# Kernel optimization log

Hardware: AMD Instinct MI355X
Metric: run time of the kernel (lower is better)

The kernel has to match this reference:

```python
import jax, jax.numpy as jnp
import numpy as np
from jax import lax


def setup_inputs() -> dict:
    key = jax.random.key(0)
    k1, k2 = jax.random.split(key)
    B, N, D = 4, 4096, 128
    f_s = jax.random.normal(k1, (B, N, D), dtype=jnp.float32)
    f_trans = jax.random.normal(k2, (B, N, D), dtype=jnp.float32)
    return {"f_s": f_s, "f_trans": f_trans}


def reference(f_s, f_trans):
    temp = 10.0
    eps = 1e-8
    B, N, D = f_s.shape
    # pairwise dot products, reused for cosine sim and for the logits ("all")
    dots = jnp.einsum('bnd,bmd->bnm', f_s, f_trans)  # [B,N,M]
    norm_s = jnp.linalg.norm(f_s, axis=-1)       # [B,N]
    norm_t = jnp.linalg.norm(f_trans, axis=-1)   # [B,M]
    # torch.cosine_similarity: dot / max(|x|*|y|, eps)
    sim = dots / jnp.maximum(norm_s[:, :, None] * norm_t[:, None, :], eps)
    # argmax over dim=1 (the N axis) -> index per (b, m)
    idx = jnp.argmax(sim, axis=1)  # [B,M] int
    # gather f_trans rows at those indices (detached in the original via numpy)
    pos_q_trans = lax.stop_gradient(
        jnp.take_along_axis(f_trans, idx[..., None], axis=1))  # [B,M,D]
    pos_logit = jnp.sum(f_s * pos_q_trans, axis=-1) / temp  # [B,N] (N==M)
    pos_exp = jnp.exp(pos_logit)
    # sum_m exp(<f_s_n, f_trans_m>/temp) without materializing [B,N,M,D]
    all_exp = jnp.sum(jnp.exp(dots / temp), axis=-1)  # [B,N]
    ratio = jnp.clip(pos_exp / all_exp, 1e-40)
    loss = jnp.mean(jnp.sum(-jnp.log(ratio), axis=-1) / N)
    return loss
```

## Files before the change

kernel.cpp:

```cpp
#include <hip/hip_runtime.h>
#include <math.h>

#define BB 4
#define NN 4096
#define DD 128
#define MSPLIT 8
#define NIT 8
#define TM 64
#define NP 128

typedef __attribute__((ext_vector_type(8))) short bf16x8;
typedef __attribute__((ext_vector_type(4))) float f32x4;

__device__ __forceinline__ void mfma_16x16x32_bf16(f32x4& d, bf16x8 a, bf16x8 b) {
  asm volatile("v_mfma_f32_16x16x32_bf16 %0, %1, %2, %0" : "+v"(d) : "v"(a), "v"(b));
}

__device__ __forceinline__ void gload16(const void* g, void* lds) {
  __builtin_amdgcn_global_load_lds(
      (const __attribute__((address_space(1))) void*)g,
      (__attribute__((address_space(3))) void*)lds, 16, 0, 0);
}

__device__ __forceinline__ unsigned short f2b(float x) {
  union { float f; unsigned u; } v; v.f = x;
  unsigned r = v.u + 0x7fffu + ((v.u >> 16) & 1u);
  return (unsigned short)(r >> 16);
}

__global__ __launch_bounds__(256) void k_prep(const float* __restrict__ fs,
                                              const float* __restrict__ ft,
                                              unsigned* __restrict__ outb,
                                              float* __restrict__ inv_norm) {
  int w = threadIdx.x >> 6, lane = threadIdx.x & 63;
  int row = blockIdx.x * 4 + w;
  bool is_s = row < BB * NN;
  const float* src = is_s ? fs + (size_t)row * DD
                          : ft + ((size_t)row - BB * NN) * DD;
  float2 v = ((const float2*)src)[lane];
  const float C = 0.14426950408889634f;
  float cx = is_s ? v.x : v.x * C;
  float cy = is_s ? v.y : v.y * C;
  outb[(size_t)row * 64 + lane] = ((unsigned)f2b(cy) << 16) | f2b(cx);
  if (is_s) {
    float s = v.x * v.x + v.y * v.y;
#pragma unroll
    for (int off = 32; off > 0; off >>= 1) s += __shfl_xor(s, off);
    if (lane == 0) inv_norm[row] = 1.0f / sqrtf(s);
  }
}

__global__ __launch_bounds__(256, 4) void k_main(const unsigned short* __restrict__ fsb,
                                                 const unsigned short* __restrict__ ftb,
                                                 const float* __restrict__ inv_norm,
                                                 float* __restrict__ psum,
                                                 float2* __restrict__ pmaxvi) {
  __shared__ __align__(16) char smem[32768];

  const int t = threadIdx.x;
  const int tn = blockIdx.x, h = blockIdx.y, b = blockIdx.z;
  const int w = t >> 6, lane = t & 63;
  const int l15 = lane & 15, g = lane >> 4;

  const int t16 = t >> 4, cp = t & 15;
  const int srcThr = t16 * 256 + ((cp ^ (t16 & 15)) << 4);
  const int ldsThr = w * 1024;

  const char* gA = (const char*)(fsb + ((size_t)b * NN + (size_t)tn * 128) * DD);
  const char* gB0 = (const char*)(ftb + ((size_t)b * NN + (size_t)h * (NIT * TM)) * DD);

#pragma unroll
  for (int p = 0; p < 8; p++)
    gload16(gA + p * 4096 + srcThr, smem + p * 4096 + ldsThr);
  __syncthreads();

  bf16x8 af[4][2];
#pragma unroll
  for (int kk = 0; kk < 4; kk++)
#pragma unroll
    for (int fi = 0; fi < 2; fi++) {
      int Ra = w * 32 + fi * 16 + l15;
      af[kk][fi] = *(const bf16x8*)(smem + Ra * 256 + (((kk * 4 + g) ^ l15) << 4));
    }
  float sv[2][4];
  int rowid[2][4];
  const float* invb = inv_norm + (size_t)b * NN + tn * 128 + w * 32 + g * 4;
#pragma unroll
  for (int fi = 0; fi < 2; fi++)
#pragma unroll
    for (int j = 0; j < 4; j++) {
      sv[fi][j] = invb[fi * 16 + j];
      rowid[fi][j] = w * 32 + fi * 16 + g * 4 + j;
    }
  __syncthreads();

  char* cb = smem;
  char* nb = smem + 16384;

#pragma unroll
  for (int p = 0; p < 4; p++)
    gload16(gB0 + p * 4096 + srcThr, cb + p * 4096 + ldsThr);

  float rowacc[2][4] = {};

  for (int it = 0; it < NIT; ++it) {
    __syncthreads();
    if (it + 1 < NIT) {
      const char* gBn = gB0 + (size_t)(it + 1) * (TM * DD * 2);
#pragma unroll
      for (int p = 0; p < 4; p++)
        gload16(gBn + p * 4096 + srcThr, nb + p * 4096 + ldsThr);
    }
    f32x4 acc[2][4] = {};
#pragma unroll
    for (int kk = 0; kk < 4; kk++) {
      bf16x8 bfr[4];
#pragma unroll
      for (int fj = 0; fj < 4; fj++) {
        int Rb = fj * 16 + l15;
        bfr[fj] = *(const bf16x8*)(cb + Rb * 256 + (((kk * 4 + g) ^ l15) << 4));
      }
#pragma unroll
      for (int fi = 0; fi < 2; fi++)
#pragma unroll
        for (int fj = 0; fj < 4; fj++)
          mfma_16x16x32_bf16(acc[fi][fj], af[kk][fi], bfr[fj]);
    }
#pragma unroll
    for (int fi = 0; fi < 2; fi++)
#pragma unroll
      for (int j = 0; j < 4; j++) {
        float s = (exp2f(acc[fi][0][j]) + exp2f(acc[fi][1][j])) +
                  (exp2f(acc[fi][2][j]) + exp2f(acc[fi][3][j]));
        rowacc[fi][j] += s;
      }
#pragma unroll
    for (int fj = 0; fj < 4; fj++) {
      float bv = -INFINITY; int bi = 0x7fffffff;
#pragma unroll
      for (int fi = 0; fi < 2; fi++)
#pragma unroll
        for (int j = 0; j < 4; j++) {
          float vv = acc[fi][fj][j] * sv[fi][j];
          if (vv > bv) { bv = vv; bi = rowid[fi][j]; }
        }
#pragma unroll
      for (int off = 16; off <= 32; off <<= 1) {
        float ov = __shfl_xor(bv, off);
        int   oi = __shfl_xor(bi, off);
        if (ov > bv || (ov == bv && oi < bi)) { bv = ov; bi = oi; }
      }
      if (g == 0) {
        int m = (h * NIT + it) * TM + fj * 16 + l15;
        float2 pr; pr.x = bv; pr.y = __int_as_float(tn * 128 + bi);
        pmaxvi[((size_t)b * NN + m) * NP + tn * 4 + w] = pr;
      }
    }
    char* tmp = cb; cb = nb; nb = tmp;
  }

#pragma unroll
  for (int fi = 0; fi < 2; fi++)
#pragma unroll
    for (int j = 0; j < 4; j++) {
      float s = rowacc[fi][j];
#pragma unroll
      for (int off = 1; off <= 8; off <<= 1) s += __shfl_xor(s, off);
      if (l15 == 0) {
        int n = tn * 128 + w * 32 + fi * 16 + g * 4 + j;
        psum[((size_t)b * NN + n) * MSPLIT + h] = s;
      }
    }
}

__global__ __launch_bounds__(256) void k_post(const float* __restrict__ fs,
                                              const float* __restrict__ ft,
                                              const float* __restrict__ psum,
                                              const float2* __restrict__ pmaxvi,
                                              float* __restrict__ blockpart) {
  __shared__ float part[4];
  int w = threadIdx.x >> 6, lane = threadIdx.x & 63;
  int row = blockIdx.x * 4 + w;
  int b = row >> 12;
  const float2* pp = pmaxvi + (size_t)row * NP;
  float2 p0 = pp[lane], p1 = pp[lane + 64];
  float v = p0.x; int i = __float_as_int(p0.y);
  {
    int i1 = __float_as_int(p1.y);
    if (p1.x > v || (p1.x == v && i1 < i)) { v = p1.x; i = i1; }
  }
#pragma unroll
  for (int off = 32; off > 0; off >>= 1) {
    float ov = __shfl_xor(v, off);
    int   oi = __shfl_xor(i, off);
    if (ov > v || (ov == v && oi < i)) { v = ov; i = oi; }
  }
  float2 a = ((const float2*)(fs + (size_t)row * DD))[lane];
  float2 c = ((const float2*)(ft + ((size_t)b * NN + i) * DD))[lane];
  float s = a.x * c.x + a.y * c.y;
#pragma unroll
  for (int off = 32; off > 0; off >>= 1) s += __shfl_xor(s, off);
  if (lane == 0) {
    const float4* ps4 = (const float4*)&psum[(size_t)row * MSPLIT];
    float4 q0 = ps4[0], q1 = ps4[1];
    float tot = ((q0.x + q0.y) + (q0.z + q0.w)) + ((q1.x + q1.y) + (q1.z + q1.w));
    float term = logf(tot) - s * 0.1f;
    part[w] = fminf(term, 92.103403719761827f);
  }
  __syncthreads();
  if (threadIdx.x == 0)
    blockpart[blockIdx.x] = part[0] + part[1] + part[2] + part[3];
}

__global__ __launch_bounds__(256) void k_final(const float* __restrict__ blockpart,
                                               float* __restrict__ out) {
  __shared__ float red[256];
  float s = 0.0f;
  for (int i = threadIdx.x; i < (BB * NN) / 4; i += 256) s += blockpart[i];
  red[threadIdx.x] = s;
  __syncthreads();
  for (int st = 128; st > 0; st >>= 1) {
    if (threadIdx.x < st) red[threadIdx.x] += red[threadIdx.x + st];
    __syncthreads();
  }
  if (threadIdx.x == 0) out[0] = red[0] * (1.0f / (BB * NN));
}

extern "C" void kernel_launch(void* const* d_in, const int* in_sizes, int n_in,
                              void* d_out, int out_size, void* d_ws, size_t ws_size,
                              hipStream_t stream) {
  const float* fs = (const float*)d_in[0];
  const float* ft = (const float*)d_in[1];
  float* out = (float*)d_out;

  const size_t NE = (size_t)BB * NN * DD;
  unsigned short* fsb = (unsigned short*)d_ws;
  unsigned short* ftb = fsb + NE;
  float*  inv_norm = (float*)(ftb + NE);
  float*  psum     = inv_norm + (size_t)BB * NN;
  float2* pmaxvi   = (float2*)(psum + (size_t)BB * NN * MSPLIT);
  float*  blockpart = (float*)(pmaxvi + (size_t)BB * NN * NP);

  k_prep<<<(2 * BB * NN) / 4, 256, 0, stream>>>(fs, ft, (unsigned*)fsb, inv_norm);
  dim3 g2(NN / 128, MSPLIT, BB);
  k_main<<<g2, 256, 0, stream>>>(fsb, ftb, inv_norm, psum, pmaxvi);
  k_post<<<(BB * NN) / 4, 256, 0, stream>>>(fs, ft, psum, pmaxvi, blockpart);
  k_final<<<1, 256, 0, stream>>>(blockpart, out);
}
```

Before: 65.76 us.

## Transpose main GEMM so argmax runs in-lane with packed index keys

Swaps the roles of the two operands so each wave owns 32 f_trans columns and scans f_s rows. The argmax over N is now a per-lane running fmax on a float key whose low 5 mantissa bits encode the tile position, which replaces the per-tile cross-lane shuffles and the wide partial-max buffer. Each wave reads operands straight from global memory without LDS staging or barriers. The exp-sum partials are written per 32-column group and reduced in the post kernel. The cost is more global and L2 traffic, no LDS reuse, and argmax ties resolved at reduced precision.

```diff
diff --git a/kernel.cpp b/kernel.cpp
--- a/kernel.cpp
+++ b/kernel.cpp
@@ -4,22 +4,15 @@
 #define BB 4
 #define NN 4096
 #define DD 128
-#define MSPLIT 8
+#define HS 8
 #define NIT 8
-#define TM 64
-#define NP 128
+#define MGROUPS 128
 
 typedef __attribute__((ext_vector_type(8))) short bf16x8;
 typedef __attribute__((ext_vector_type(4))) float f32x4;
 
 __device__ __forceinline__ void mfma_16x16x32_bf16(f32x4& d, bf16x8 a, bf16x8 b) {
   asm volatile("v_mfma_f32_16x16x32_bf16 %0, %1, %2, %0" : "+v"(d) : "v"(a), "v"(b));
-}
-
-__device__ __forceinline__ void gload16(const void* g, void* lds) {
-  __builtin_amdgcn_global_load_lds(
-      (const __attribute__((address_space(1))) void*)g,
-      (__attribute__((address_space(3))) void*)lds, 16, 0, 0);
 }
 
 __device__ __forceinline__ unsigned short f2b(float x) {
@@ -38,9 +31,8 @@
   const float* src = is_s ? fs + (size_t)row * DD
                           : ft + ((size_t)row - BB * NN) * DD;
   float2 v = ((const float2*)src)[lane];
-  const float C = 0.14426950408889634f;
-  float cx = is_s ? v.x : v.x * C;
-  float cy = is_s ? v.y : v.y * C;
+  float cx = is_s ? v.x : v.x * 0.1f;
+  float cy = is_s ? v.y : v.y * 0.1f;
   outb[(size_t)row * 64 + lane] = ((unsigned)f2b(cy) << 16) | f2b(cx);
   if (is_s) {
     float s = v.x * v.x + v.y * v.y;
@@ -54,121 +46,101 @@
                                                  const unsigned short* __restrict__ ftb,
                                                  const float* __restrict__ inv_norm,
                                                  float* __restrict__ psum,
-                                                 float2* __restrict__ pmaxvi) {
-  __shared__ __align__(16) char smem[32768];
-
+                                                 float2* __restrict__ pmax) {
   const int t = threadIdx.x;
-  const int tn = blockIdx.x, h = blockIdx.y, b = blockIdx.z;
   const int w = t >> 6, lane = t & 63;
   const int l15 = lane & 15, g = lane >> 4;
-
-  const int t16 = t >> 4, cp = t & 15;
-  const int srcThr = t16 * 256 + ((cp ^ (t16 & 15)) << 4);
-  const int ldsThr = w * 1024;
-
-  const char* gA = (const char*)(fsb + ((size_t)b * NN + (size_t)tn * 128) * DD);
-  const char* gB0 = (const char*)(ftb + ((size_t)b * NN + (size_t)h * (NIT * TM)) * DD);
-
-#pragma unroll
-  for (int p = 0; p < 8; p++)
-    gload16(gA + p * 4096 + srcThr, smem + p * 4096 + ldsThr);
-  __syncthreads();
-
+  const int gw = blockIdx.x * 4 + w;
+  const int b = gw >> 10;
+  const int h = (gw >> 7) & 7;
+  const int mg = gw & 127;
+  const int m0 = mg * 32;
+
+  const unsigned short* Abase = ftb + ((size_t)b * NN + m0) * DD;
   bf16x8 af[4][2];
 #pragma unroll
   for (int kk = 0; kk < 4; kk++)
 #pragma unroll
-    for (int fi = 0; fi < 2; fi++) {
-      int Ra = w * 32 + fi * 16 + l15;
-      af[kk][fi] = *(const bf16x8*)(smem + Ra * 256 + (((kk * 4 + g) ^ l15) << 4));
-    }
-  float sv[2][4];
-  int rowid[2][4];
-  const float* invb = inv_norm + (size_t)b * NN + tn * 128 + w * 32 + g * 4;
-#pragma unroll
-  for (int fi = 0; fi < 2; fi++)
+    for (int mf = 0; mf < 2; mf++)
+      af[kk][mf] = *(const bf16x8*)(Abase + (mf * 16 + l15) * DD + kk * 32 + g * 8);
+
+  const unsigned short* Ball = fsb + (size_t)b * NN * DD;
+  const float* invb = inv_norm + (size_t)b * NN;
+
+  float bkey[2][4];
+#pragma unroll
+  for (int mf = 0; mf < 2; mf++)
+#pragma unroll
+    for (int j = 0; j < 4; j++) bkey[mf][j] = 0.0f;
+
+#pragma unroll 1
+  for (int it = 0; it < NIT; ++it) {
+    const int n0 = h * 512 + it * 64;
+    float svn[4];
+#pragma unroll
+    for (int fj = 0; fj < 4; fj++) svn[fj] = invb[n0 + fj * 16 + l15];
+
+    f32x4 acc[2][4] = {};
+#pragma unroll
+    for (int kk = 0; kk < 4; kk++) {
+      bf16x8 bf[4];
+#pragma unroll
+      for (int fj = 0; fj < 4; fj++)
+        bf[fj] = *(const bf16x8*)(Ball + (size_t)(n0 + fj * 16 + l15) * DD + kk * 32 + g * 8);
+#pragma unroll
+      for (int mf = 0; mf < 2; mf++)
+#pragma unroll
+        for (int fj = 0; fj < 4; fj++)
+          mfma_16x16x32_bf16(acc[mf][fj], af[kk][mf], bf[fj]);
+    }
+
+#pragma unroll
+    for (int fj = 0; fj < 4; fj++) {
+      float s = (__expf(acc[0][fj][0]) + __expf(acc[0][fj][1])) +
+                (__expf(acc[0][fj][2]) + __expf(acc[0][fj][3])) +
+                (__expf(acc[1][fj][0]) + __expf(acc[1][fj][1])) +
+                (__expf(acc[1][fj][2]) + __expf(acc[1][fj][3]));
+      s += __shfl_xor(s, 16);
+      s += __shfl_xor(s, 32);
+      if (g == 0)
+        psum[((size_t)b * NN + n0 + fj * 16 + l15) * MGROUPS + mg] = s;
+    }
+
+    const unsigned codebase = (unsigned)((7 - it) << 2);
+#pragma unroll
+    for (int fj = 0; fj < 4; fj++) {
+      const unsigned code = codebase | (unsigned)(3 - fj);
+#pragma unroll
+      for (int mf = 0; mf < 2; mf++)
+#pragma unroll
+        for (int j = 0; j < 4; j++) {
+          float v = fmaf(acc[mf][fj][j], svn[fj], 4.0f);
+          unsigned kb = (__float_as_uint(v) & 0xFFFFFFE0u) | code;
+          bkey[mf][j] = fmaxf(bkey[mf][j], __uint_as_float(kb));
+        }
+    }
+  }
+
+#pragma unroll
+  for (int mf = 0; mf < 2; mf++)
 #pragma unroll
     for (int j = 0; j < 4; j++) {
-      sv[fi][j] = invb[fi * 16 + j];
-      rowid[fi][j] = w * 32 + fi * 16 + g * 4 + j;
-    }
-  __syncthreads();
-
-  char* cb = smem;
-  char* nb = smem + 16384;
-
-#pragma unroll
-  for (int p = 0; p < 4; p++)
-    gload16(gB0 + p * 4096 + srcThr, cb + p * 4096 + ldsThr);
-
-  float rowacc[2][4] = {};
-
-  for (int it = 0; it < NIT; ++it) {
-    __syncthreads();
-    if (it + 1 < NIT) {
-      const char* gBn = gB0 + (size_t)(it + 1) * (TM * DD * 2);
-#pragma unroll
-      for (int p = 0; p < 4; p++)
-        gload16(gBn + p * 4096 + srcThr, nb + p * 4096 + ldsThr);
-    }
-    f32x4 acc[2][4] = {};
-#pragma unroll
-    for (int kk = 0; kk < 4; kk++) {
-      bf16x8 bfr[4];
-#pragma unroll
-      for (int fj = 0; fj < 4; fj++) {
-        int Rb = fj * 16 + l15;
-        bfr[fj] = *(const bf16x8*)(cb + Rb * 256 + (((kk * 4 + g) ^ l15) << 4));
+      unsigned bits = __float_as_uint(bkey[mf][j]);
+      unsigned code = bits & 31u;
+      int itw = 7 - (int)(code >> 2);
+      int fjw = 3 - (int)(code & 3u);
+      int n = h * 512 + itw * 64 + fjw * 16 + l15;
+      float vq = __uint_as_float(bits & 0xFFFFFFE0u);
+#pragma unroll
+      for (int off = 1; off <= 8; off <<= 1) {
+        float ov = __shfl_xor(vq, off);
+        int   on = __shfl_xor(n, off);
+        if (ov > vq || (ov == vq && on < n)) { vq = ov; n = on; }
       }
-#pragma unroll
-      for (int fi = 0; fi < 2; fi++)
-#pragma unroll
-        for (int fj = 0; fj < 4; fj++)
-          mfma_16x16x32_bf16(acc[fi][fj], af[kk][fi], bfr[fj]);
-    }
-#pragma unroll
-    for (int fi = 0; fi < 2; fi++)
-#pragma unroll
-      for (int j = 0; j < 4; j++) {
-        float s = (exp2f(acc[fi][0][j]) + exp2f(acc[fi][1][j])) +
-                  (exp2f(acc[fi][2][j]) + exp2f(acc[fi][3][j]));
-        rowacc[fi][j] += s;
-      }
-#pragma unroll
-    for (int fj = 0; fj < 4; fj++) {
-      float bv = -INFINITY; int bi = 0x7fffffff;
-#pragma unroll
-      for (int fi = 0; fi < 2; fi++)
-#pragma unroll
-        for (int j = 0; j < 4; j++) {
-          float vv = acc[fi][fj][j] * sv[fi][j];
-          if (vv > bv) { bv = vv; bi = rowid[fi][j]; }
-        }
-#pragma unroll
-      for (int off = 16; off <= 32; off <<= 1) {
-        float ov = __shfl_xor(bv, off);
-        int   oi = __shfl_xor(bi, off);
-        if (ov > bv || (ov == bv && oi < bi)) { bv = ov; bi = oi; }
-      }
-      if (g == 0) {
-        int m = (h * NIT + it) * TM + fj * 16 + l15;
-        float2 pr; pr.x = bv; pr.y = __int_as_float(tn * 128 + bi);
-        pmaxvi[((size_t)b * NN + m) * NP + tn * 4 + w] = pr;
-      }
-    }
-    char* tmp = cb; cb = nb; nb = tmp;
-  }
-
-#pragma unroll
-  for (int fi = 0; fi < 2; fi++)
-#pragma unroll
-    for (int j = 0; j < 4; j++) {
-      float s = rowacc[fi][j];
-#pragma unroll
-      for (int off = 1; off <= 8; off <<= 1) s += __shfl_xor(s, off);
       if (l15 == 0) {
-        int n = tn * 128 + w * 32 + fi * 16 + g * 4 + j;
-        psum[((size_t)b * NN + n) * MSPLIT + h] = s;
+        int m = m0 + mf * 16 + g * 4 + j;
+        float2 pr; pr.x = vq; pr.y = __int_as_float(n);
+        pmax[((size_t)b * NN + m) * HS + h] = pr;
       }
     }
 }
@@ -176,34 +148,34 @@
 __global__ __launch_bounds__(256) void k_post(const float* __restrict__ fs,
                                               const float* __restrict__ ft,
                                               const float* __restrict__ psum,
-                                              const float2* __restrict__ pmaxvi,
+                                              const float2* __restrict__ pmax,
                                               float* __restrict__ blockpart) {
   __shared__ float part[4];
   int w = threadIdx.x >> 6, lane = threadIdx.x & 63;
   int row = blockIdx.x * 4 + w;
   int b = row >> 12;
-  const float2* pp = pmaxvi + (size_t)row * NP;
-  float2 p0 = pp[lane], p1 = pp[lane + 64];
-  float v = p0.x; int i = __float_as_int(p0.y);
-  {
-    int i1 = __float_as_int(p1.y);
-    if (p1.x > v || (p1.x == v && i1 < i)) { v = p1.x; i = i1; }
-  }
-#pragma unroll
-  for (int off = 32; off > 0; off >>= 1) {
+  float v = -INFINITY; int i = 0x7fffffff;
+  if (lane < HS) {
+    float2 pm = pmax[(size_t)row * HS + lane];
+    v = pm.x; i = __float_as_int(pm.y);
+  }
+#pragma unroll
+  for (int off = 1; off <= 4; off <<= 1) {
     float ov = __shfl_xor(v, off);
     int   oi = __shfl_xor(i, off);
     if (ov > v || (ov == v && oi < i)) { v = ov; i = oi; }
   }
+  int j = __shfl(i, 0);
+  float2 q = ((const float2*)(psum + (size_t)row * MGROUPS))[lane];
+  float tot = q.x + q.y;
+#pragma unroll
+  for (int off = 32; off > 0; off >>= 1) tot += __shfl_xor(tot, off);
   float2 a = ((const float2*)(fs + (size_t)row * DD))[lane];
-  float2 c = ((const float2*)(ft + ((size_t)b * NN + i) * DD))[lane];
+  float2 c = ((const float2*)(ft + ((size_t)b * NN + j) * DD))[lane];
   float s = a.x * c.x + a.y * c.y;
 #pragma unroll
   for (int off = 32; off > 0; off >>= 1) s += __shfl_xor(s, off);
   if (lane == 0) {
-    const float4* ps4 = (const float4*)&psum[(size_t)row * MSPLIT];
-    float4 q0 = ps4[0], q1 = ps4[1];
-    float tot = ((q0.x + q0.y) + (q0.z + q0.w)) + ((q1.x + q1.y) + (q1.z + q1.w));
     float term = logf(tot) - s * 0.1f;
     part[w] = fminf(term, 92.103403719761827f);
   }
@@ -238,12 +210,11 @@
   unsigned short* ftb = fsb + NE;
   float*  inv_norm = (float*)(ftb + NE);
   float*  psum     = inv_norm + (size_t)BB * NN;
-  float2* pmaxvi   = (float2*)(psum + (size_t)BB * NN * MSPLIT);
-  float*  blockpart = (float*)(pmaxvi + (size_t)BB * NN * NP);
+  float2* pmax     = (float2*)(psum + (size_t)BB * NN * MGROUPS);
+  float*  blockpart = (float*)(pmax + (size_t)BB * NN * HS);
 
   k_prep<<<(2 * BB * NN) / 4, 256, 0, stream>>>(fs, ft, (unsigned*)fsb, inv_norm);
-  dim3 g2(NN / 128, MSPLIT, BB);
-  k_main<<<g2, 256, 0, stream>>>(fsb, ftb, inv_norm, psum, pmaxvi);
-  k_post<<<(BB * NN) / 4, 256, 0, stream>>>(fs, ft, psum, pmaxvi, blockpart);
+  k_main<<<(BB * HS * MGROUPS) / 4, 256, 0, stream>>>(fsb, ftb, inv_norm, psum, pmax);
+  k_post<<<(BB * NN) / 4, 256, 0, stream>>>(fs, ft, psum, pmax, blockpart);
   k_final<<<1, 256, 0, stream>>>(blockpart, out);
 }
```

After: 96.07 us. 46.1% more time.
